# Optimization experiments

Hardware: AMD Instinct MI355X
Metric: run time of the kernel (lower is better)

Reference implementation:

```python
import jax, jax.numpy as jnp
import numpy as np
import math

EMBED_SIZE = 2048
HEADS = 32
GROUPS = 8
HEAD_DIM = EMBED_SIZE // HEADS          # 64
HPG = HEADS // GROUPS                   # heads per group = 4
N, L = 4, 1024


def setup_inputs() -> dict:
    key = jax.random.key(0)
    k1, k2, k3, k4, k5 = jax.random.split(key, 5)
    values = jax.random.normal(k1, (N, L, EMBED_SIZE), dtype=jnp.float32)
    keys = jax.random.normal(k2, (N, L, EMBED_SIZE), dtype=jnp.float32)
    queries = jax.random.normal(k3, (N, L, EMBED_SIZE), dtype=jnp.float32)
    mask = jnp.ones((N, 1, 1, L, L), dtype=jnp.int32)
    # fc_out: Linear(heads*head_dim -> embed_size), torch default init ~ U(-1/sqrt(in), 1/sqrt(in))
    bound = 1.0 / math.sqrt(EMBED_SIZE)
    W_out = jax.random.uniform(k4, (EMBED_SIZE, EMBED_SIZE), jnp.float32, -bound, bound)
    b_out = jax.random.uniform(k5, (EMBED_SIZE,), jnp.float32, -bound, bound)
    return {"values": values, "keys": keys, "queries": queries, "mask": mask,
            "W_out": W_out, "b_out": b_out}


def reference(values, keys, queries, mask, W_out, b_out):
    n, q_len, _ = queries.shape
    k_len = keys.shape[1]
    # split into (N, L, groups, heads_per_group, head_dim)
    v = values.reshape(n, k_len, GROUPS, HPG, HEAD_DIM)
    k = keys.reshape(n, k_len, GROUPS, HPG, HEAD_DIM)
    q = queries.reshape(n, q_len, GROUPS, HPG, HEAD_DIM)
    # scores: (N, groups, heads_per_group, q, k)
    energy = jnp.einsum('nqghd,nkghd->nghqk', q, k)
    energy = jnp.where(mask == 0, jnp.float32(-1e20), energy)
    attn = jax.nn.softmax(energy / jnp.sqrt(jnp.float32(EMBED_SIZE)), axis=-1)
    out = jnp.einsum('nghqk,nkghd->nqghd', attn, v).reshape(n, q_len, EMBED_SIZE)
    return out @ W_out.T + b_out
```

## Files before the change

### kernel.cpp

```cpp
#include <hip/hip_runtime.h>
#include <math.h>


#define LSEQ 1024
#define EMB  2048

typedef __bf16 bf16x8 __attribute__((ext_vector_type(8)));
typedef float floatx4 __attribute__((ext_vector_type(4)));
typedef unsigned short ushort8v __attribute__((ext_vector_type(8)));

__device__ __forceinline__ float4 ld4(const float* p) { return *(const float4*)p; }

__device__ __forceinline__ unsigned short f2bf(float x) {
    unsigned u = __float_as_uint(x);
    u += 0x7FFFu + ((u >> 16) & 1u);
    return (unsigned short)(u >> 16);
}

__device__ __forceinline__ void gl_lds16(const void* g, void* l) {
    __builtin_amdgcn_global_load_lds((const __attribute__((address_space(1))) void*)g,
                                     (__attribute__((address_space(3))) void*)l, 16, 0, 0);
}

__device__ __forceinline__ void stage64(const unsigned short* g, size_t gstride,
                                        unsigned short* lds) {
    const int t = threadIdx.x;
    #pragma unroll
    for (int h = 0; h < 2; h++) {
        const int idx = h * 256 + t;
        const int r   = idx >> 3;
        const int sl  = (idx & 7) ^ (r & 7);
        gl_lds16(g + (size_t)r * gstride + sl * 8, lds + idx * 8);
    }
}

__device__ __forceinline__ bf16x8 frag_ld(const unsigned short* lds, int row, int seg) {
    return *(const bf16x8*)(lds + row * 64 + ((seg ^ (row & 7)) * 8));
}

__global__ __launch_bounds__(256)
void cvt_bf16(const float* __restrict__ x, unsigned short* __restrict__ y) {
    const size_t i = ((size_t)blockIdx.x * 256 + threadIdx.x) * 8;
    float4 a = ld4(x + i), b = ld4(x + i + 4);
    ushort8v h;
    h[0] = f2bf(a.x); h[1] = f2bf(a.y); h[2] = f2bf(a.z); h[3] = f2bf(a.w);
    h[4] = f2bf(b.x); h[5] = f2bf(b.y); h[6] = f2bf(b.z); h[7] = f2bf(b.w);
    *(ushort8v*)(y + i) = h;
}

__global__ __launch_bounds__(256)
void prep_vt(const float* __restrict__ V, unsigned short* __restrict__ Vt) {
    __shared__ float tile[64][68];
    const int bid = blockIdx.x;
    const int kc = bid & 15, h = (bid >> 4) & 31, n = bid >> 9;
    const int t = threadIdx.x;
    {
        const int rr = t >> 2, c4 = (t & 3) * 16;
        const float* src = V + ((size_t)(n * LSEQ + kc * 64 + rr)) * EMB + h * 64 + c4;
        #pragma unroll
        for (int j = 0; j < 4; j++)
            *(float4*)&tile[rr][c4 + j * 4] = ld4(src + j * 4);
    }
    __syncthreads();
    const int d = t >> 2, k16 = (t & 3) * 16;
    unsigned short* dst = Vt + ((size_t)((n * 32 + h) * 64 + d)) * 1024 + kc * 64 + k16;
    ushort8v o0, o1;
    #pragma unroll
    for (int j = 0; j < 8; j++) o0[j] = f2bf(tile[k16 + j][d]);
    #pragma unroll
    for (int j = 0; j < 8; j++) o1[j] = f2bf(tile[k16 + 8 + j][d]);
    *(ushort8v*)dst = o0;
    *(ushort8v*)(dst + 8) = o1;
}

#define PSTR 72
__global__ __launch_bounds__(256, 4)
void gqa_attn_mfma(const float* __restrict__ Qf, const unsigned short* __restrict__ Kh,
                   const unsigned short* __restrict__ Vt, unsigned short* __restrict__ Ah) {
    __shared__ unsigned short sQ[64 * 64];
    __shared__ unsigned short sK[64 * 64];
    __shared__ unsigned short sV[64 * 64];
    __shared__ unsigned short sP[64 * PSTR];

    const int bid  = blockIdx.x;
    const int qt   = bid & 15;
    const int head = (bid >> 4) & 31;
    const int n    = bid >> 9;
    const int q0   = qt * 64;

    const int t = threadIdx.x, w = t >> 6, lane = t & 63;
    const int lm = lane & 15, cq = lane >> 4;
    const int w16 = w * 16;

    const float scale = 0.022097086912079612f;

    const unsigned short* Kb = Kh + ((size_t)(n * LSEQ)) * EMB + head * 64;
    const unsigned short* Vb = Vt + ((size_t)(n * 32 + head)) * 64 * 1024;

    #pragma unroll
    for (int h = 0; h < 2; h++) {
        const int idx = h * 256 + t;
        const int r = idx >> 3;
        const int sl = idx & 7;
        const int sp = sl ^ (r & 7);
        const float* src = Qf + ((size_t)(n * LSEQ + q0 + r)) * EMB + head * 64 + sl * 8;
        float4 x0 = ld4(src), x1 = ld4(src + 4);
        float xs[8] = {x0.x, x0.y, x0.z, x0.w, x1.x, x1.y, x1.z, x1.w};
        ushort8v hv;
        #pragma unroll
        for (int j = 0; j < 8; j++) hv[j] = f2bf(xs[j] * scale);
        *(ushort8v*)(sQ + r * 64 + sp * 8) = hv;
    }
    __syncthreads();

    bf16x8 qf[2];
    #pragma unroll
    for (int hf = 0; hf < 2; hf++) qf[hf] = frag_ld(sQ, w16 + lm, hf * 4 + cq);

    floatx4 o[4];
    #pragma unroll
    for (int dt = 0; dt < 4; dt++) o[dt] = (floatx4){0.f, 0.f, 0.f, 0.f};
    float lpart = 0.f;

    for (int kc = 0; kc < 16; kc++) {
        __syncthreads();
        stage64(Kb + (size_t)(kc * 64) * EMB, EMB, sK);
        stage64(Vb + kc * 64, 1024, sV);
        __syncthreads();

        floatx4 s[4];
        #pragma unroll
        for (int kt = 0; kt < 4; kt++) s[kt] = (floatx4){0.f, 0.f, 0.f, 0.f};
        #pragma unroll
        for (int kt = 0; kt < 4; kt++) {
            #pragma unroll
            for (int hf = 0; hf < 2; hf++) {
                bf16x8 kf = frag_ld(sK, kt * 16 + lm, hf * 4 + cq);
                s[kt] = __builtin_amdgcn_mfma_f32_16x16x32_bf16(kf, qf[hf], s[kt], 0, 0, 0);
            }
        }

        #pragma unroll
        for (int kt = 0; kt < 4; kt++) {
            float p[4];
            #pragma unroll
            for (int r = 0; r < 4; r++) { p[r] = __expf(s[kt][r]); lpart += p[r]; }
            ushort4 pk;
            pk.x = f2bf(p[0]); pk.y = f2bf(p[1]); pk.z = f2bf(p[2]); pk.w = f2bf(p[3]);
            *(ushort4*)(sP + (w16 + lm) * PSTR + kt * 16 + cq * 4) = pk;
        }

        #pragma unroll
        for (int hf = 0; hf < 2; hf++) {
            bf16x8 pf = *(const bf16x8*)(sP + (w16 + lm) * PSTR + hf * 32 + cq * 8);
            #pragma unroll
            for (int dt = 0; dt < 4; dt++) {
                bf16x8 vf = frag_ld(sV, dt * 16 + lm, hf * 4 + cq);
                o[dt] = __builtin_amdgcn_mfma_f32_16x16x32_bf16(pf, vf, o[dt], 0, 0, 0);
            }
        }
    }

    float lred = lpart;
    lred += __shfl_xor(lred, 16);
    lred += __shfl_xor(lred, 32);

    const size_t obase = ((size_t)(n * LSEQ + q0 + w16 + cq * 4)) * EMB + head * 64 + lm;
    #pragma unroll
    for (int r = 0; r < 4; r++) {
        const float inv = 1.f / __shfl(lred, cq * 4 + r);
        #pragma unroll
        for (int dt = 0; dt < 4; dt++)
            Ah[obase + (size_t)r * EMB + dt * 16] = f2bf(o[dt][r] * inv);
    }
}

__global__ __launch_bounds__(256, 4)
void out_proj_bf16(const unsigned short* __restrict__ A, const unsigned short* __restrict__ B,
                   const float* __restrict__ bias, float* __restrict__ C) {
    __shared__ unsigned short sA[128 * 32];
    __shared__ unsigned short sB[64 * 32];

    const int t = threadIdx.x, bid = blockIdx.x;
    const int nb = bid & 31, mb = bid >> 5;
    const int m0 = mb * 128, n0 = nb * 64;
    const int wave = t >> 6, lane = t & 63;
    const int wr = wave >> 1, wc = wave & 1;
    const int lm = lane & 15, cq = lane >> 4;
    const int sw = (lm & 3) ^ ((lm >> 2) & 3);

    floatx4 acc[4][2];
    #pragma unroll
    for (int i = 0; i < 4; i++)
        #pragma unroll
        for (int j = 0; j < 2; j++)
            acc[i][j] = (floatx4){0.f, 0.f, 0.f, 0.f};

    for (int kc = 0; kc < 64; kc++) {
        __syncthreads();
        #pragma unroll
        for (int h = 0; h < 2; h++) {
            const int idx = h * 256 + t;
            const int r = idx >> 2;
            const int sl = (idx & 3) ^ (r & 3) ^ ((r >> 2) & 3);
            gl_lds16(A + (size_t)(m0 + r) * 2048 + kc * 32 + sl * 8, sA + idx * 8);
        }
        {
            const int r = t >> 2;
            const int sl = (t & 3) ^ (r & 3) ^ ((r >> 2) & 3);
            gl_lds16(B + (size_t)(n0 + r) * 2048 + kc * 32 + sl * 8, sB + t * 8);
        }
        __syncthreads();

        bf16x8 af[4], bf[2];
        #pragma unroll
        for (int i = 0; i < 4; i++)
            af[i] = *(const bf16x8*)(sA + (wr * 64 + i * 16 + lm) * 32 + ((cq ^ sw) * 8));
        #pragma unroll
        for (int j = 0; j < 2; j++)
            bf[j] = *(const bf16x8*)(sB + (wc * 32 + j * 16 + lm) * 32 + ((cq ^ sw) * 8));
        #pragma unroll
        for (int i = 0; i < 4; i++)
            #pragma unroll
            for (int j = 0; j < 2; j++)
                acc[i][j] = __builtin_amdgcn_mfma_f32_16x16x32_bf16(af[i], bf[j], acc[i][j], 0, 0, 0);
    }

    const int lr = cq * 4;
    #pragma unroll
    for (int j = 0; j < 2; j++) {
        const int col = n0 + wc * 32 + j * 16 + lm;
        const float bv = bias[col];
        #pragma unroll
        for (int i = 0; i < 4; i++) {
            const int rowb = m0 + wr * 64 + i * 16 + lr;
            #pragma unroll
            for (int r = 0; r < 4; r++)
                C[(size_t)(rowb + r) * 2048 + col] = acc[i][j][r] + bv;
        }
    }
}

extern "C" void kernel_launch(void* const* d_in, const int* in_sizes, int n_in,
                              void* d_out, int out_size, void* d_ws, size_t ws_size,
                              hipStream_t stream) {
    const float* V = (const float*)d_in[0];
    const float* K = (const float*)d_in[1];
    const float* Q = (const float*)d_in[2];
    const float* W = (const float*)d_in[4];
    const float* b = (const float*)d_in[5];
    float* out = (float*)d_out;

    unsigned short* Ah = (unsigned short*)d_ws;
    unsigned short* Kh = Ah + (size_t)4096 * 2048;
    unsigned short* Vt = Kh + (size_t)4096 * 2048;
    unsigned short* Wh = Kh;

    cvt_bf16<<<4096, 256, 0, stream>>>(K, Kh);
    prep_vt<<<2048, 256, 0, stream>>>(V, Vt);
    gqa_attn_mfma<<<2048, 256, 0, stream>>>(Q, Kh, Vt, Ah);
    cvt_bf16<<<2048, 256, 0, stream>>>(W, Wh);
    out_proj_bf16<<<1024, 256, 0, stream>>>(Ah, Wh, b, out);
}
```

Baseline: 280.4 us.

## Fuse prep kernels, double attention query tile, widen out-proj K tile

Merges the K convert, W convert and V transpose kernels into one launch, with W written to its own workspace region. Each attention block now handles 128 queries so every staged K/V tile feeds twice the MFMA work; the log2(e) factor is folded into the query scale so exp2 can be used, and occupancy drops to 3 blocks. The output projection stages 64-wide K chunks with the shared swizzled stager, halving the loop trip count and barriers. In exchange the kernels use more LDS and registers, and the attention launch has half as many blocks.

```diff
diff --git a/kernel.cpp b/kernel.cpp
--- a/kernel.cpp
+++ b/kernel.cpp
@@ -34,71 +34,93 @@
     }
 }
 
+__device__ __forceinline__ void stage128(const unsigned short* g, size_t gstride,
+                                         unsigned short* lds) {
+    const int t = threadIdx.x;
+    #pragma unroll
+    for (int h = 0; h < 4; h++) {
+        const int idx = h * 256 + t;
+        const int r   = idx >> 3;
+        const int sl  = (idx & 7) ^ (r & 7);
+        gl_lds16(g + (size_t)r * gstride + sl * 8, lds + idx * 8);
+    }
+}
+
 __device__ __forceinline__ bf16x8 frag_ld(const unsigned short* lds, int row, int seg) {
     return *(const bf16x8*)(lds + row * 64 + ((seg ^ (row & 7)) * 8));
 }
 
 __global__ __launch_bounds__(256)
-void cvt_bf16(const float* __restrict__ x, unsigned short* __restrict__ y) {
-    const size_t i = ((size_t)blockIdx.x * 256 + threadIdx.x) * 8;
-    float4 a = ld4(x + i), b = ld4(x + i + 4);
-    ushort8v h;
-    h[0] = f2bf(a.x); h[1] = f2bf(a.y); h[2] = f2bf(a.z); h[3] = f2bf(a.w);
-    h[4] = f2bf(b.x); h[5] = f2bf(b.y); h[6] = f2bf(b.z); h[7] = f2bf(b.w);
-    *(ushort8v*)(y + i) = h;
-}
-
-__global__ __launch_bounds__(256)
-void prep_vt(const float* __restrict__ V, unsigned short* __restrict__ Vt) {
+void prep_all(const float* __restrict__ K, unsigned short* __restrict__ Kh,
+              const float* __restrict__ W, unsigned short* __restrict__ Wh,
+              const float* __restrict__ V, unsigned short* __restrict__ Vt) {
     __shared__ float tile[64][68];
     const int bid = blockIdx.x;
-    const int kc = bid & 15, h = (bid >> 4) & 31, n = bid >> 9;
     const int t = threadIdx.x;
-    {
-        const int rr = t >> 2, c4 = (t & 3) * 16;
-        const float* src = V + ((size_t)(n * LSEQ + kc * 64 + rr)) * EMB + h * 64 + c4;
-        #pragma unroll
-        for (int j = 0; j < 4; j++)
-            *(float4*)&tile[rr][c4 + j * 4] = ld4(src + j * 4);
-    }
-    __syncthreads();
-    const int d = t >> 2, k16 = (t & 3) * 16;
-    unsigned short* dst = Vt + ((size_t)((n * 32 + h) * 64 + d)) * 1024 + kc * 64 + k16;
-    ushort8v o0, o1;
-    #pragma unroll
-    for (int j = 0; j < 8; j++) o0[j] = f2bf(tile[k16 + j][d]);
-    #pragma unroll
-    for (int j = 0; j < 8; j++) o1[j] = f2bf(tile[k16 + 8 + j][d]);
-    *(ushort8v*)dst = o0;
-    *(ushort8v*)(dst + 8) = o1;
-}
-
-#define PSTR 72
-__global__ __launch_bounds__(256, 4)
+    if (bid < 4096) {
+        const size_t i = ((size_t)bid * 256 + t) * 8;
+        float4 a = ld4(K + i), b = ld4(K + i + 4);
+        ushort8v h;
+        h[0] = f2bf(a.x); h[1] = f2bf(a.y); h[2] = f2bf(a.z); h[3] = f2bf(a.w);
+        h[4] = f2bf(b.x); h[5] = f2bf(b.y); h[6] = f2bf(b.z); h[7] = f2bf(b.w);
+        *(ushort8v*)(Kh + i) = h;
+    } else if (bid < 6144) {
+        const size_t i = ((size_t)(bid - 4096) * 256 + t) * 8;
+        float4 a = ld4(W + i), b = ld4(W + i + 4);
+        ushort8v h;
+        h[0] = f2bf(a.x); h[1] = f2bf(a.y); h[2] = f2bf(a.z); h[3] = f2bf(a.w);
+        h[4] = f2bf(b.x); h[5] = f2bf(b.y); h[6] = f2bf(b.z); h[7] = f2bf(b.w);
+        *(ushort8v*)(Wh + i) = h;
+    } else {
+        const int vb = bid - 6144;
+        const int kc = vb & 15, h = (vb >> 4) & 31, n = vb >> 9;
+        {
+            const int rr = t >> 2, c4 = (t & 3) * 16;
+            const float* src = V + ((size_t)(n * LSEQ + kc * 64 + rr)) * EMB + h * 64 + c4;
+            #pragma unroll
+            for (int j = 0; j < 4; j++)
+                *(float4*)&tile[rr][c4 + j * 4] = ld4(src + j * 4);
+        }
+        __syncthreads();
+        const int d = t >> 2, k16 = (t & 3) * 16;
+        unsigned short* dst = Vt + ((size_t)((n * 32 + h) * 64 + d)) * 1024 + kc * 64 + k16;
+        ushort8v o0, o1;
+        #pragma unroll
+        for (int j = 0; j < 8; j++) o0[j] = f2bf(tile[k16 + j][d]);
+        #pragma unroll
+        for (int j = 0; j < 8; j++) o1[j] = f2bf(tile[k16 + 8 + j][d]);
+        *(ushort8v*)dst = o0;
+        *(ushort8v*)(dst + 8) = o1;
+    }
+}
+
+#define PSTR 76
+__global__ __launch_bounds__(256, 3)
 void gqa_attn_mfma(const float* __restrict__ Qf, const unsigned short* __restrict__ Kh,
                    const unsigned short* __restrict__ Vt, unsigned short* __restrict__ Ah) {
-    __shared__ unsigned short sQ[64 * 64];
+    __shared__ unsigned short sQ[128 * 64];
     __shared__ unsigned short sK[64 * 64];
     __shared__ unsigned short sV[64 * 64];
-    __shared__ unsigned short sP[64 * PSTR];
+    __shared__ unsigned short sP[128 * PSTR];
 
     const int bid  = blockIdx.x;
-    const int qt   = bid & 15;
-    const int head = (bid >> 4) & 31;
-    const int n    = bid >> 9;
-    const int q0   = qt * 64;
+    const int hl   = bid & 127;
+    const int qt   = bid >> 7;
+    const int head = hl & 31;
+    const int n    = hl >> 5;
+    const int q0   = qt * 128;
 
     const int t = threadIdx.x, w = t >> 6, lane = t & 63;
     const int lm = lane & 15, cq = lane >> 4;
-    const int w16 = w * 16;
-
-    const float scale = 0.022097086912079612f;
+    const int w32 = w * 32;
+
+    const float scale2 = 0.03187936190857805f;
 
     const unsigned short* Kb = Kh + ((size_t)(n * LSEQ)) * EMB + head * 64;
     const unsigned short* Vb = Vt + ((size_t)(n * 32 + head)) * 64 * 1024;
 
     #pragma unroll
-    for (int h = 0; h < 2; h++) {
+    for (int h = 0; h < 4; h++) {
         const int idx = h * 256 + t;
         const int r = idx >> 3;
         const int sl = idx & 7;
@@ -108,19 +130,24 @@
         float xs[8] = {x0.x, x0.y, x0.z, x0.w, x1.x, x1.y, x1.z, x1.w};
         ushort8v hv;
         #pragma unroll
-        for (int j = 0; j < 8; j++) hv[j] = f2bf(xs[j] * scale);
+        for (int j = 0; j < 8; j++) hv[j] = f2bf(xs[j] * scale2);
         *(ushort8v*)(sQ + r * 64 + sp * 8) = hv;
     }
     __syncthreads();
 
-    bf16x8 qf[2];
-    #pragma unroll
-    for (int hf = 0; hf < 2; hf++) qf[hf] = frag_ld(sQ, w16 + lm, hf * 4 + cq);
-
-    floatx4 o[4];
-    #pragma unroll
-    for (int dt = 0; dt < 4; dt++) o[dt] = (floatx4){0.f, 0.f, 0.f, 0.f};
-    float lpart = 0.f;
+    bf16x8 qf[2][2];
+    #pragma unroll
+    for (int set = 0; set < 2; set++)
+        #pragma unroll
+        for (int hf = 0; hf < 2; hf++)
+            qf[set][hf] = frag_ld(sQ, w32 + set * 16 + lm, hf * 4 + cq);
+
+    floatx4 o[2][4];
+    #pragma unroll
+    for (int set = 0; set < 2; set++)
+        #pragma unroll
+        for (int dt = 0; dt < 4; dt++) o[set][dt] = (floatx4){0.f, 0.f, 0.f, 0.f};
+    float lpart[2] = {0.f, 0.f};
 
     for (int kc = 0; kc < 16; kc++) {
         __syncthreads();
@@ -128,58 +155,72 @@
         stage64(Vb + kc * 64, 1024, sV);
         __syncthreads();
 
-        floatx4 s[4];
-        #pragma unroll
-        for (int kt = 0; kt < 4; kt++) s[kt] = (floatx4){0.f, 0.f, 0.f, 0.f};
+        floatx4 s[2][4];
+        #pragma unroll
+        for (int set = 0; set < 2; set++)
+            #pragma unroll
+            for (int kt = 0; kt < 4; kt++) s[set][kt] = (floatx4){0.f, 0.f, 0.f, 0.f};
         #pragma unroll
         for (int kt = 0; kt < 4; kt++) {
             #pragma unroll
             for (int hf = 0; hf < 2; hf++) {
                 bf16x8 kf = frag_ld(sK, kt * 16 + lm, hf * 4 + cq);
-                s[kt] = __builtin_amdgcn_mfma_f32_16x16x32_bf16(kf, qf[hf], s[kt], 0, 0, 0);
+                s[0][kt] = __builtin_amdgcn_mfma_f32_16x16x32_bf16(kf, qf[0][hf], s[0][kt], 0, 0, 0);
+                s[1][kt] = __builtin_amdgcn_mfma_f32_16x16x32_bf16(kf, qf[1][hf], s[1][kt], 0, 0, 0);
             }
         }
 
         #pragma unroll
-        for (int kt = 0; kt < 4; kt++) {
-            float p[4];
-            #pragma unroll
-            for (int r = 0; r < 4; r++) { p[r] = __expf(s[kt][r]); lpart += p[r]; }
-            ushort4 pk;
-            pk.x = f2bf(p[0]); pk.y = f2bf(p[1]); pk.z = f2bf(p[2]); pk.w = f2bf(p[3]);
-            *(ushort4*)(sP + (w16 + lm) * PSTR + kt * 16 + cq * 4) = pk;
+        for (int set = 0; set < 2; set++) {
+            #pragma unroll
+            for (int kt = 0; kt < 4; kt++) {
+                float p[4];
+                #pragma unroll
+                for (int r = 0; r < 4; r++) {
+                    p[r] = __builtin_amdgcn_exp2f(s[set][kt][r]);
+                    lpart[set] += p[r];
+                }
+                ushort4 pk;
+                pk.x = f2bf(p[0]); pk.y = f2bf(p[1]); pk.z = f2bf(p[2]); pk.w = f2bf(p[3]);
+                *(ushort4*)(sP + (w32 + set * 16 + lm) * PSTR + kt * 16 + cq * 4) = pk;
+            }
         }
 
         #pragma unroll
         for (int hf = 0; hf < 2; hf++) {
-            bf16x8 pf = *(const bf16x8*)(sP + (w16 + lm) * PSTR + hf * 32 + cq * 8);
+            bf16x8 pf0 = *(const bf16x8*)(sP + (w32 + lm) * PSTR + hf * 32 + cq * 8);
+            bf16x8 pf1 = *(const bf16x8*)(sP + (w32 + 16 + lm) * PSTR + hf * 32 + cq * 8);
             #pragma unroll
             for (int dt = 0; dt < 4; dt++) {
                 bf16x8 vf = frag_ld(sV, dt * 16 + lm, hf * 4 + cq);
-                o[dt] = __builtin_amdgcn_mfma_f32_16x16x32_bf16(pf, vf, o[dt], 0, 0, 0);
+                o[0][dt] = __builtin_amdgcn_mfma_f32_16x16x32_bf16(pf0, vf, o[0][dt], 0, 0, 0);
+                o[1][dt] = __builtin_amdgcn_mfma_f32_16x16x32_bf16(pf1, vf, o[1][dt], 0, 0, 0);
             }
         }
     }
 
-    float lred = lpart;
-    lred += __shfl_xor(lred, 16);
-    lred += __shfl_xor(lred, 32);
-
-    const size_t obase = ((size_t)(n * LSEQ + q0 + w16 + cq * 4)) * EMB + head * 64 + lm;
-    #pragma unroll
-    for (int r = 0; r < 4; r++) {
-        const float inv = 1.f / __shfl(lred, cq * 4 + r);
-        #pragma unroll
-        for (int dt = 0; dt < 4; dt++)
-            Ah[obase + (size_t)r * EMB + dt * 16] = f2bf(o[dt][r] * inv);
+    #pragma unroll
+    for (int set = 0; set < 2; set++) {
+        float lred = lpart[set];
+        lred += __shfl_xor(lred, 16);
+        lred += __shfl_xor(lred, 32);
+        const size_t obase =
+            ((size_t)(n * LSEQ + q0 + w32 + set * 16 + cq * 4)) * EMB + head * 64 + lm;
+        #pragma unroll
+        for (int r = 0; r < 4; r++) {
+            const float inv = 1.f / __shfl(lred, cq * 4 + r);
+            #pragma unroll
+            for (int dt = 0; dt < 4; dt++)
+                Ah[obase + (size_t)r * EMB + dt * 16] = f2bf(o[set][dt][r] * inv);
+        }
     }
 }
 
 __global__ __launch_bounds__(256, 4)
 void out_proj_bf16(const unsigned short* __restrict__ A, const unsigned short* __restrict__ B,
                    const float* __restrict__ bias, float* __restrict__ C) {
-    __shared__ unsigned short sA[128 * 32];
-    __shared__ unsigned short sB[64 * 32];
+    __shared__ unsigned short sA[128 * 64];
+    __shared__ unsigned short sB[64 * 64];
 
     const int t = threadIdx.x, bid = blockIdx.x;
     const int nb = bid & 31, mb = bid >> 5;
@@ -187,7 +228,6 @@
     const int wave = t >> 6, lane = t & 63;
     const int wr = wave >> 1, wc = wave & 1;
     const int lm = lane & 15, cq = lane >> 4;
-    const int sw = (lm & 3) ^ ((lm >> 2) & 3);
 
     floatx4 acc[4][2];
     #pragma unroll
@@ -196,34 +236,31 @@
         for (int j = 0; j < 2; j++)
             acc[i][j] = (floatx4){0.f, 0.f, 0.f, 0.f};
 
-    for (int kc = 0; kc < 64; kc++) {
-        __syncthreads();
-        #pragma unroll
-        for (int h = 0; h < 2; h++) {
-            const int idx = h * 256 + t;
-            const int r = idx >> 2;
-            const int sl = (idx & 3) ^ (r & 3) ^ ((r >> 2) & 3);
-            gl_lds16(A + (size_t)(m0 + r) * 2048 + kc * 32 + sl * 8, sA + idx * 8);
-        }
-        {
-            const int r = t >> 2;
-            const int sl = (t & 3) ^ (r & 3) ^ ((r >> 2) & 3);
-            gl_lds16(B + (size_t)(n0 + r) * 2048 + kc * 32 + sl * 8, sB + t * 8);
-        }
-        __syncthreads();
-
-        bf16x8 af[4], bf[2];
+    for (int kc = 0; kc < 32; kc++) {
+        __syncthreads();
+        stage128(A + (size_t)m0 * 2048 + kc * 64, 2048, sA);
+        stage64(B + (size_t)n0 * 2048 + kc * 64, 2048, sB);
+        __syncthreads();
+
+        bf16x8 af[4][2], bf[2][2];
         #pragma unroll
         for (int i = 0; i < 4; i++)
-            af[i] = *(const bf16x8*)(sA + (wr * 64 + i * 16 + lm) * 32 + ((cq ^ sw) * 8));
+            #pragma unroll
+            for (int kk = 0; kk < 2; kk++)
+                af[i][kk] = frag_ld(sA, wr * 64 + i * 16 + lm, kk * 4 + cq);
         #pragma unroll
         for (int j = 0; j < 2; j++)
-            bf[j] = *(const bf16x8*)(sB + (wc * 32 + j * 16 + lm) * 32 + ((cq ^ sw) * 8));
+            #pragma unroll
+            for (int kk = 0; kk < 2; kk++)
+                bf[j][kk] = frag_ld(sB, wc * 32 + j * 16 + lm, kk * 4 + cq);
         #pragma unroll
         for (int i = 0; i < 4; i++)
             #pragma unroll
             for (int j = 0; j < 2; j++)
-                acc[i][j] = __builtin_amdgcn_mfma_f32_16x16x32_bf16(af[i], bf[j], acc[i][j], 0, 0, 0);
+                #pragma unroll
+                for (int kk = 0; kk < 2; kk++)
+                    acc[i][j] = __builtin_amdgcn_mfma_f32_16x16x32_bf16(af[i][kk], bf[j][kk],
+                                                                        acc[i][j], 0, 0, 0);
     }
 
     const int lr = cq * 4;
@@ -254,11 +291,11 @@
     unsigned short* Ah = (unsigned short*)d_ws;
     unsigned short* Kh = Ah + (size_t)4096 * 2048;
     unsigned short* Vt = Kh + (size_t)4096 * 2048;
-    unsigned short* Wh = Kh;
-
-    cvt_bf16<<<4096, 256, 0, stream>>>(K, Kh);
-    prep_vt<<<2048, 256, 0, stream>>>(V, Vt);
-    gqa_attn_mfma<<<2048, 256, 0, stream>>>(Q, Kh, Vt, Ah);
-    cvt_bf16<<<2048, 256, 0, stream>>>(W, Wh);
-    out_proj_bf16<<<1024, 256, 0, stream>>>(Ah, Wh, b, out);
-}
+    unsigned short* Wh = Ah;
+    unsigned short* Wh2 = Vt + (size_t)4 * 32 * 64 * 1024;
+
+    prep_all<<<8192, 256, 0, stream>>>(K, Kh, W, Wh2, V, Vt);
+    gqa_attn_mfma<<<1024, 256, 0, stream>>>(Q, Kh, Vt, Ah);
+    out_proj_bf16<<<1024, 256, 0, stream>>>(Ah, Wh2, b, out);
+    (void)Wh;
+}
```

New measurement: 259.3 us. -7.5%, faster.
